# Kernel optimization log

Hardware: AMD Instinct MI355X
Metric: run time of the kernel (lower is better)

## Reference

```python
import math
import jax, jax.numpy as jnp
import numpy as np
from jax import lax

PI = math.pi

def _gauss1d(ks, sigma):
    # kornia gaussian: centered at (ks-1)/2 for both odd and even ks
    x = jnp.arange(ks, dtype=jnp.float32) - (ks - 1) / 2.0
    g = jnp.exp(-0.5 * (x / sigma) ** 2)
    return g / g.sum()

def _unfold_nonoverlap(x, k):
    # F.unfold(x, kernel_size=k, stride=k) for x (B,1,H,W), H,W divisible by k
    B, C, H, W = x.shape
    nH, nW = H // k, W // k
    p = x.reshape(B, nH, k, nW, k).transpose(0, 2, 4, 1, 3)
    return p.reshape(B, k * k, nH * nW)

def _sift(x, ps, nab=8, nsb=4, clipval=0.2, eps=1e-10):
    # kornia SIFTDescriptor(patch_size=ps), x: (N,1,ps,ps) -> (N,128)
    N = x.shape[0]
    g1 = _gauss1d(ps, ps / math.sqrt(2.0))
    gk = jnp.outer(g1, g1)  # (ps,ps), sum 1
    # spatial_gradient mode='diff', normalized, replicate pad
    xp = jnp.pad(x, ((0, 0), (0, 0), (0, 0), (1, 1)), mode='edge')
    gx = 0.5 * (xp[..., 2:] - xp[..., :-2])
    yp = jnp.pad(x, ((0, 0), (0, 0), (1, 1), (0, 0)), mode='edge')
    gy = 0.5 * (yp[:, :, 2:, :] - yp[:, :, :-2, :])
    mag = jnp.sqrt(gx * gx + gy * gy + eps) * gk  # (N,1,ps,ps)
    ori = jnp.arctan2(gy, gx + eps) + 2.0 * PI
    o_big = nab * ori / (2.0 * PI)
    bo0f = jnp.floor(o_big)
    w1 = o_big - bo0f
    bo0 = bo0f.astype(jnp.int32) % nab
    bo1 = (bo0 + 1) % nab
    c0 = jax.nn.one_hot(bo0[:, 0], nab, axis=1, dtype=x.dtype)  # (N,8,ps,ps)
    c1 = jax.nn.one_hot(bo1[:, 0], nab, axis=1, dtype=x.dtype)
    bins = c0 * ((1.0 - w1) * mag) + c1 * (w1 * mag)  # (N,8,ps,ps)
    # triangular pooling kernel, depthwise conv over the 8 angular bins
    bk = 2 * (ps // (nsb + 1)); stride = ps // nsb; pad = bk // 4
    half = bk / 2.0
    xc2 = half - jnp.abs(jnp.arange(bk, dtype=jnp.float32) + 0.5 - half)
    pk = jnp.outer(xc2, xc2) / (half * half)
    pk = jnp.tile(pk[None, None], (nab, 1, 1, 1))  # (8,1,bk,bk)
    pooled = lax.conv_general_dilated(bins, pk, (stride, stride),
        [(pad, pad), (pad, pad)], feature_group_count=nab,
        dimension_numbers=('NCHW', 'OIHW', 'NCHW'))  # (N,8,4,4)
    d = pooled.reshape(N, -1)
    d = d / jnp.maximum(jnp.linalg.norm(d, axis=1, keepdims=True), 1e-12)
    d = jnp.clip(d, 0.0, clipval)
    d = d / jnp.maximum(jnp.linalg.norm(d, axis=1, keepdims=True), 1e-12)
    d = jnp.sqrt(d / jnp.maximum(jnp.abs(d).sum(1, keepdims=True), 1e-12) + eps)  # rootsift
    return d

def _conv_t(x, w, b, stride=2, pad=1):
    # torch ConvTranspose2d; w: (Cin,Cout,k,k)
    k = w.shape[-1]
    wT = jnp.transpose(jnp.flip(w, (-2, -1)), (1, 0, 2, 3))  # (Cout,Cin,k,k)
    y = lax.conv_general_dilated(x, wT, (1, 1),
        [(k - 1 - pad, k - 1 - pad)] * 2, lhs_dilation=(stride, stride),
        dimension_numbers=('NCHW', 'OIHW', 'NCHW'))
    return y + b[None, :, None, None]

def _gn(x, groups, w, b, eps=1e-5):
    N, C, H, W = x.shape
    xg = x.reshape(N, groups, -1)
    mean = xg.mean(-1, keepdims=True)
    var = ((xg - mean) ** 2).mean(-1, keepdims=True)
    xn = ((xg - mean) * lax.rsqrt(var + eps)).reshape(N, C, H, W)
    return xn * w[None, :, None, None] + b[None, :, None, None]

def _jbf(x, guide, ky, kx, sigma_color, sy, sx):
    # kornia joint_bilateral_blur, border='reflect', color_distance='l1'
    B, C, H, W = x.shape
    py, px = ky // 2, kx // 2
    xp = jnp.pad(x, ((0, 0), (0, 0), (py, py), (px, px)), mode='reflect')
    gp = jnp.pad(guide, ((0, 0), (0, 0), (py, py), (px, px)), mode='reflect')
    def win(p):
        return jnp.stack([p[:, :, i:i + H, j:j + W] for i in range(ky) for j in range(kx)], axis=-1)
    ux, ug = win(xp), win(gp)  # (B,C,H,W,ky*kx)
    diff = ug - guide[..., None]
    cd2 = jnp.square(jnp.sum(jnp.abs(diff), axis=1, keepdims=True))
    ck = jnp.exp((-0.5 / (sigma_color ** 2)) * cd2)  # (B,1,H,W,K)
    sk = jnp.outer(_gauss1d(ky, sy), _gauss1d(kx, sx)).reshape(1, 1, 1, 1, -1)
    kern = sk * ck
    return (ux * kern).sum(-1) / kern.sum(-1)

def _forward(x, d1w, d1b, g1w, g1b, s1w, s1b, d2w, d2b, g2w, g2b, s2w, s2b,
             d3w, d3b, g3w, g3b, d4w, d4b, g4w, g4b, fw, fb):
    B = x.shape[0]
    s7 = _sift(_unfold_nonoverlap(x, 7).reshape(-1, 1, 32, 32), 32).reshape(B, 128, 7, 7)
    h = jax.nn.relu(_gn(_conv_t(s7, d1w, d1b), 8, g1w, g1b))  # (B,32,14,14); dropout=identity (eval)
    s14 = _sift(_unfold_nonoverlap(x, 14).reshape(-1, 1, 16, 16), 16).reshape(B, 128, 14, 14)
    sk1 = jnp.einsum('bchw,oc->bohw', s14, s1w[:, :, 0, 0]) + s1b[None, :, None, None]
    h = jax.nn.relu(_gn(_conv_t(jnp.concatenate([h, sk1], 1), d2w, d2b), 4, g2w, g2b))  # (B,16,28,28)
    s28 = _sift(_unfold_nonoverlap(x, 28).reshape(-1, 1, 8, 8), 8).reshape(B, 128, 28, 28)
    sk2 = jnp.einsum('bchw,oc->bohw', s28, s2w[:, :, 0, 0]) + s2b[None, :, None, None]
    h = jax.nn.relu(_gn(_conv_t(jnp.concatenate([h, sk2], 1), d3w, d3b), 2, g3w, g3b))  # (B,8,56,56)
    h = jax.nn.relu(_gn(_conv_t(h, d4w, d4b), 1, g4w, g4b))  # (B,4,112,112)
    h = _conv_t(h, fw, fb)  # (B,2,224,224)
    h = _jbf(h, jnp.tile(x, (1, 2, 1, 1)), 5, 5, 0.1, 1.5, 1.5)
    scale = jnp.array([0.436, 0.615], dtype=h.dtype)
    return jnp.tanh(h) * scale[None, :, None, None]

def setup_inputs() -> dict:
    key = jax.random.key(0)
    ks = jax.random.split(key, 8)
    B = 16
    f32 = jnp.float32
    def rn(k, shp, s=0.05):
        return jax.random.normal(k, shp, f32) * s
    return {
        'x': jax.random.uniform(ks[0], (B, 1, 224, 224), f32),
        'd1w': rn(ks[1], (128, 32, 4, 4)), 'd1b': jnp.zeros((32,), f32),
        'g1w': jnp.ones((32,), f32), 'g1b': jnp.zeros((32,), f32),
        's1w': rn(ks[2], (32, 128, 1, 1)), 's1b': jnp.zeros((32,), f32),
        'd2w': rn(ks[3], (64, 16, 4, 4)), 'd2b': jnp.zeros((16,), f32),
        'g2w': jnp.ones((16,), f32), 'g2b': jnp.zeros((16,), f32),
        's2w': rn(ks[4], (16, 128, 1, 1)), 's2b': jnp.zeros((16,), f32),
        'd3w': rn(ks[5], (32, 8, 4, 4)), 'd3b': jnp.zeros((8,), f32),
        'g3w': jnp.ones((8,), f32), 'g3b': jnp.zeros((8,), f32),
        'd4w': rn(ks[6], (8, 4, 4, 4)), 'd4b': jnp.zeros((4,), f32),
        'g4w': jnp.ones((4,), f32), 'g4b': jnp.zeros((4,), f32),
        'fw': rn(ks[7], (4, 2, 4, 4)), 'fb': jnp.zeros((2,), f32),
    }

def reference(x, d1w, d1b, g1w, g1b, s1w, s1b, d2w, d2b, g2w, g2b, s2w, s2b,
              d3w, d3b, g3w, g3b, d4w, d4b, g4w, g4b, fw, fb):
    return _forward(x, d1w, d1b, g1w, g1b, s1w, s1b, d2w, d2b, g2w, g2b, s2w, s2b,
                    d3w, d3b, g3w, g3b, d4w, d4b, g4w, g4b, fw, fb)
```

## Files before the change

kernel.cpp:

```cpp
#include <hip/hip_runtime.h>
#include <math.h>

#define PI_F 3.14159265358979323846f

template<int PS, int K, int NT>
__global__ __launch_bounds__(NT)
void sift_kernel(const float* __restrict__ x, float* __restrict__ out)
{
    constexpr int NPIX = PS*PS;
    constexpr int BK = 2*(PS/5);
    constexpr int STRIDE = PS/4;
    constexpr int PAD = BK/4;
    constexpr float HALF = BK*0.5f;

    __shared__ float patch[NPIX];
    __shared__ float bins[8*NPIX];
    __shared__ float g1[PS];
    __shared__ float desc[128];
    __shared__ float red[NT];
    __shared__ float gsum_s;

    const int tid = threadIdx.x;
    const int n = blockIdx.x;
    const int b = n / (K*K);
    const int c = n % (K*K);
    const int ki = c / K;
    const int kj = c % K;

    const float* xb = x + (size_t)b*224*224;
    for (int idx = tid; idx < NPIX; idx += NT) {
        int i = idx / PS, j = idx - i*PS;
        patch[idx] = xb[(i*K + ki)*224 + (j*K + kj)];
    }
    if (tid < PS) {
        const float sigma = (float)PS * 0.70710678118654752440f;
        float xv = (float)tid - (PS-1)*0.5f;
        float t = xv / sigma;
        g1[tid] = expf(-0.5f*t*t);
    }
    for (int idx = tid; idx < 8*NPIX; idx += NT) bins[idx] = 0.f;
    __syncthreads();
    if (tid == 0) {
        float s = 0.f;
        for (int i = 0; i < PS; i++) s += g1[i];
        gsum_s = s;
    }
    __syncthreads();
    const float ginv = 1.0f / (gsum_s*gsum_s);

    for (int idx = tid; idx < NPIX; idx += NT) {
        int i = idx / PS, j = idx - i*PS;
        int jm = j > 0 ? j-1 : 0, jp = j < PS-1 ? j+1 : PS-1;
        int im = i > 0 ? i-1 : 0, ip = i < PS-1 ? i+1 : PS-1;
        float gx = 0.5f*(patch[i*PS+jp] - patch[i*PS+jm]);
        float gy = 0.5f*(patch[ip*PS+j] - patch[im*PS+j]);
        float mag = sqrtf(gx*gx + gy*gy + 1e-10f) * (g1[i]*g1[j]*ginv);
        float ori = atan2f(gy, gx + 1e-10f) + 2.f*PI_F;
        float obig = ori * (8.f/(2.f*PI_F));
        float bo0f = floorf(obig);
        float w1 = obig - bo0f;
        int bo0 = ((int)bo0f) & 7;
        int bo1 = (bo0 + 1) & 7;
        bins[bo0*NPIX + idx] = (1.f - w1)*mag;
        bins[bo1*NPIX + idx] = w1*mag;
    }
    __syncthreads();

    for (int t = tid; t < 128; t += NT) {
        int o = t >> 4;
        int py = (t >> 2) & 3;
        int px = t & 3;
        int sy = py*STRIDE - PAD;
        int sx = px*STRIDE - PAD;
        const float* bo = bins + o*NPIX;
        float acc = 0.f;
        for (int di = 0; di < BK; di++) {
            int i = sy + di;
            if (i < 0 || i >= PS) continue;
            float wi = HALF - fabsf((float)di + 0.5f - HALF);
            for (int dj = 0; dj < BK; dj++) {
                int j = sx + dj;
                if (j < 0 || j >= PS) continue;
                float wj = HALF - fabsf((float)dj + 0.5f - HALF);
                acc += bo[i*PS + j] * (wi*wj);
            }
        }
        desc[t] = acc * (1.0f/(HALF*HALF));
    }
    __syncthreads();

    float d = (tid < 128) ? desc[tid] : 0.f;
    red[tid] = d*d; __syncthreads();
    for (int s = NT/2; s > 0; s >>= 1) { if (tid < s) red[tid] += red[tid+s]; __syncthreads(); }
    float nrm = sqrtf(red[0]); __syncthreads();
    d = d / fmaxf(nrm, 1e-12f);
    d = fminf(fmaxf(d, 0.f), 0.2f);
    red[tid] = d*d; __syncthreads();
    for (int s = NT/2; s > 0; s >>= 1) { if (tid < s) red[tid] += red[tid+s]; __syncthreads(); }
    nrm = sqrtf(red[0]); __syncthreads();
    d = d / fmaxf(nrm, 1e-12f);
    red[tid] = d; __syncthreads();
    for (int s = NT/2; s > 0; s >>= 1) { if (tid < s) red[tid] += red[tid+s]; __syncthreads(); }
    float ssum = red[0];
    d = sqrtf(d / fmaxf(ssum, 1e-12f) + 1e-10f);
    if (tid < 128) out[(size_t)n*128 + tid] = d;
}

template<int CIN0, int CIN1, int COUT, int G, int HIN, int NCH, int RT, int NT,
         bool FUSE, int GIN, int NGIN, int NBLK_IN, int NBLK_OUT>
__global__ __launch_bounds__(NT)
void convt_tiled(const float* __restrict__ in0, const float* __restrict__ in1,
                 const float* __restrict__ w, const float* __restrict__ bias,
                 const float2* __restrict__ pst_in,
                 const float* __restrict__ gnw, const float* __restrict__ gnb,
                 float* __restrict__ out, float2* __restrict__ pst_out)
{
    constexpr int CIN = CIN0 + CIN1;
    constexpr int CG = COUT / G;
    constexpr int NGRP = NCH / CG;
    constexpr int CB = COUT / NCH;
    constexpr int H0 = 2*HIN;
    constexpr int SP = H0*H0;
    constexpr int HIN2 = HIN*HIN;
    constexpr int NR = RT/2 + 2;
    constexpr int WIN = HIN + 2;
    constexpr int TILE = CIN*NR*WIN;
    constexpr int WSTRIDE = CIN*NCH*4 + 4;
    constexpr int NPOS = RT*H0;
    constexpr int NWAVE = NT/64;

    __shared__ float tile[TILE];
    __shared__ float wl2[4*WSTRIDE];
    __shared__ float a_s[CIN0];
    __shared__ float b_s[CIN0];
    __shared__ float wpart[NWAVE][NGRP][2];

    const int tid = threadIdx.x;
    const int by = blockIdx.y;
    const int bx = blockIdx.x;
    const int b  = by / CB;
    const int cb = by - b*CB;
    const int c0 = cb*NCH;
    const int g0 = c0 / CG;
    const int r0 = bx * RT;
    const int row0 = r0/2 - 1;

    if constexpr (FUSE) {
        if (tid < CIN0) {
            int gi = tid / (CIN0/GIN);
            float s0 = 0.f, s1 = 0.f;
            for (int k = 0; k < NBLK_IN; k++) {
                float2 p = pst_in[((size_t)b*GIN + gi)*NBLK_IN + k];
                s0 += p.x; s1 += p.y;
            }
            float mean = s0 * (1.f/NGIN);
            float var  = s1 * (1.f/NGIN) - mean*mean;
            float inv  = rsqrtf(var + 1e-5f);
            float a = inv * gnw[tid];
            a_s[tid] = a;
            b_s[tid] = gnb[tid] - mean*a;
        }
        __syncthreads();
    }

    for (int idx = tid; idx < 4*CIN*NCH*4; idx += NT) {
        int k = idx & 3;
        int t2 = idx >> 2;
        int j = t2 % NCH; t2 /= NCH;
        int ci = t2 % CIN;
        int pq = t2 / CIN;
        int pA = pq >> 1, qA = pq & 1;
        int dy = pA + 2*(k>>1), dx = qA + 2*(k&1);
        wl2[pq*WSTRIDE + (ci*NCH + j)*4 + k] = w[(ci*COUT + c0 + j)*16 + dy*4 + dx];
    }

    const float* i0 = in0 + (size_t)b*CIN0*HIN2;
    for (int idx = tid; idx < TILE; idx += NT) {
        int c = idx % WIN;
        int t2 = idx / WIN;
        int r = t2 % NR;
        int ci = t2 / NR;
        int iy = row0 + r, ix = c - 1;
        float v = 0.f;
        if (iy >= 0 && iy < HIN && ix >= 0 && ix < HIN) {
            if (CIN1 == 0 || ci < CIN0) {
                v = i0[ci*HIN2 + iy*HIN + ix];
                if constexpr (FUSE) v = fmaxf(v*a_s[ci] + b_s[ci], 0.f);
            } else {
                v = in1[((size_t)b*CIN1 + (ci-CIN0))*HIN2 + iy*HIN + ix];
            }
        }
        tile[idx] = v;
    }
    __syncthreads();

    float acc[NCH];
    #pragma unroll
    for (int j = 0; j < NCH; j++) acc[j] = 0.f;

    const bool active = tid < NPOS;
    if (active) {
        int oy = r0 + tid / H0, ox = tid % H0;
        int pA = (oy+1)&1, qA = (ox+1)&1;
        int iyA = (oy+1-pA)>>1, ixA = (ox+1-qA)>>1;
        int rA = iyA - row0;
        int cA = ixA + 1;
        int toff = rA*WIN + cA;
        const float* wbase = wl2 + (pA*2+qA)*WSTRIDE;

        #pragma unroll
        for (int j = 0; j < NCH; j++) acc[j] = bias[c0 + j];

        #pragma unroll 4
        for (int ci = 0; ci < CIN; ci++) {
            const float* tp = tile + ci*(NR*WIN) + toff;
            float l0 = tp[0];
            float l1 = tp[-1];
            float l2 = tp[-WIN];
            float l3 = tp[-WIN-1];
            const float* wr = wbase + ci*NCH*4;
            #pragma unroll
            for (int j = 0; j < NCH; j++) {
                const float4 wv = *(const float4*)(wr + j*4);
                acc[j] += l0*wv.x + l1*wv.y + l2*wv.z + l3*wv.w;
            }
        }
        float* ob = out + ((size_t)b*COUT + c0)*SP + r0*H0 + tid;
        #pragma unroll
        for (int j = 0; j < NCH; j++) ob[j*SP] = acc[j];
    }

    const int wv = tid >> 6;
    const int ln = tid & 63;
    #pragma unroll
    for (int grp = 0; grp < NGRP; grp++) {
        float ps = 0.f, pq2 = 0.f;
        #pragma unroll
        for (int j = 0; j < CG; j++) {
            float v = active ? acc[grp*CG + j] : 0.f;
            ps += v; pq2 += v*v;
        }
        #pragma unroll
        for (int off = 32; off > 0; off >>= 1) {
            ps  += __shfl_down(ps,  off);
            pq2 += __shfl_down(pq2, off);
        }
        if (ln == 0) { wpart[wv][grp][0] = ps; wpart[wv][grp][1] = pq2; }
    }
    __syncthreads();
    if (tid < NGRP) {
        float s0 = 0.f, s1 = 0.f;
        #pragma unroll
        for (int w2 = 0; w2 < NWAVE; w2++) { s0 += wpart[w2][tid][0]; s1 += wpart[w2][tid][1]; }
        pst_out[((size_t)b*G + g0 + tid)*NBLK_OUT + bx] = make_float2(s0, s1);
    }
}

template<int CO, int S>
__global__ __launch_bounds__(256)
void conv1x1(const float* __restrict__ in, const float* __restrict__ w,
             const float* __restrict__ bias, float* __restrict__ out)
{
    __shared__ float wt[128*CO];
    const int tid = threadIdx.x;
    for (int i = tid; i < 128*CO; i += 256) {
        int c = i / CO, co = i - c*CO;
        wt[i] = w[co*128 + c];
    }
    __syncthreads();
    int idx = blockIdx.x*256 + tid;
    int s = idx % S; int r = idx / S;
    int co4 = r % (CO/4); int b = r / (CO/4);
    int co = co4*4;
    const float* ib = in + (size_t)b*128*S + s;
    float acc0 = bias[co], acc1 = bias[co+1], acc2 = bias[co+2], acc3 = bias[co+3];
    #pragma unroll 8
    for (int c = 0; c < 128; c++) {
        float v = ib[c*S];
        const float4 wv = *(const float4*)&wt[c*CO + co];
        acc0 += v*wv.x; acc1 += v*wv.y; acc2 += v*wv.z; acc3 += v*wv.w;
    }
    float* ob = out + ((size_t)b*CO + co)*S + s;
    ob[0] = acc0; ob[S] = acc1; ob[2*S] = acc2; ob[3*S] = acc3;
}

__global__ __launch_bounds__(256)
void convt_final_fused(const float* __restrict__ in, const float* __restrict__ w,
                       const float* __restrict__ bias,
                       const float2* __restrict__ pst_in,
                       const float* __restrict__ gnw, const float* __restrict__ gnb,
                       float* __restrict__ out)
{
    __shared__ float wl2[128];
    __shared__ float a_s[4], b_s[4], bl[2], mv[2];
    const int tid = threadIdx.x;
    const int b = blockIdx.y;
    if (tid < 128) {
        int k = tid & 3;
        int t = tid >> 2;
        int co = t & 1; t >>= 1;
        int ci = t & 3;
        int pq = t >> 2;
        int pA = pq >> 1, qA = pq & 1;
        int dy = pA + 2*(k>>1), dx = qA + 2*(k&1);
        wl2[tid] = w[(ci*2 + co)*16 + dy*4 + dx];
    }
    if (tid < 2) bl[tid] = bias[tid];
    if (tid < 64) {
        float s0 = 0.f, s1 = 0.f;
        for (int k = tid; k < 56; k += 64) {
            float2 p = pst_in[(size_t)b*56 + k];
            s0 += p.x; s1 += p.y;
        }
        #pragma unroll
        for (int off = 32; off > 0; off >>= 1) {
            s0 += __shfl_down(s0, off);
            s1 += __shfl_down(s1, off);
        }
        if (tid == 0) {
            float mean = s0 * (1.f/50176.f);
            float var  = s1 * (1.f/50176.f) - mean*mean;
            mv[0] = mean;
            mv[1] = rsqrtf(var + 1e-5f);
        }
    }
    __syncthreads();
    if (tid < 4) {
        float a = mv[1] * gnw[tid];
        a_s[tid] = a;
        b_s[tid] = gnb[tid] - mv[0]*a;
    }
    __syncthreads();

    int e = blockIdx.x*256 + tid;
    int oy = e / 224, ox = e - oy*224;
    int pA = (oy+1)&1, iyA = (oy+1-pA)>>1, iyB = iyA-1;
    int qA = (ox+1)&1, ixA = (ox+1-qA)>>1, ixB = ixA-1;
    float mYA = (iyA < 112) ? 1.f : 0.f;
    float mYB = (iyB >= 0)  ? 1.f : 0.f;
    float mXA = (ixA < 112) ? 1.f : 0.f;
    float mXB = (ixB >= 0)  ? 1.f : 0.f;
    float m0 = mYA*mXA, m1 = mYA*mXB, m2 = mYB*mXA, m3 = mYB*mXB;
    int iyAc = min(iyA, 111), iyBc = max(iyB, 0);
    int ixAc = min(ixA, 111), ixBc = max(ixB, 0);
    int oAA = iyAc*112 + ixAc, oAB = iyAc*112 + ixBc;
    int oBA = iyBc*112 + ixAc, oBB = iyBc*112 + ixBc;
    const float* wbase = wl2 + (pA*2+qA)*32;

    float acc0 = bl[0], acc1 = bl[1];
    const float* ib = in + (size_t)b*4*112*112;
    #pragma unroll
    for (int ci = 0; ci < 4; ci++) {
        const float* ip = ib + ci*112*112;
        float a = a_s[ci], bb = b_s[ci];
        float l0 = fmaxf(ip[oAA]*a + bb, 0.f);
        float l1 = fmaxf(ip[oAB]*a + bb, 0.f);
        float l2 = fmaxf(ip[oBA]*a + bb, 0.f);
        float l3 = fmaxf(ip[oBB]*a + bb, 0.f);
        float t0 = l0*m0, t1 = l1*m1, t2 = l2*m2, t3 = l3*m3;
        const float4 w0 = *(const float4*)(wbase + ci*8);
        const float4 w1 = *(const float4*)(wbase + ci*8 + 4);
        acc0 += t0*w0.x + t1*w0.y + t2*w0.z + t3*w0.w;
        acc1 += t0*w1.x + t1*w1.y + t2*w1.z + t3*w1.w;
    }
    float* ob = out + (size_t)b*2*50176 + e;
    ob[0] = acc0;
    ob[50176] = acc1;
}

__global__ __launch_bounds__(256)
void bilateral_tanh(const float* __restrict__ x, const float* __restrict__ pre,
                    float* __restrict__ out)
{
    const float g[5] = {0.1200783f, 0.2338817f, 0.2920800f, 0.2338817f, 0.1200783f};
    int idx = blockIdx.x*256 + threadIdx.x;
    int px = idx % 224; int r = idx / 224;
    int py = r % 224; int b = r / 224;
    int s = py*224 + px;
    const float* xb = x + (size_t)b*50176;
    const float* p0 = pre + (size_t)b*2*50176;
    const float* p1 = p0 + 50176;
    float center = xb[s];
    float wsum = 0.f, a0 = 0.f, a1 = 0.f;
    #pragma unroll
    for (int di = -2; di <= 2; di++){
        int yy = py + di; yy = yy < 0 ? -yy : (yy > 223 ? 446 - yy : yy);
        #pragma unroll
        for (int dj = -2; dj <= 2; dj++){
            int xx = px + dj; xx = xx < 0 ? -xx : (xx > 223 ? 446 - xx : xx);
            int o = yy*224 + xx;
            float dg = xb[o] - center;
            float wgt = g[di+2]*g[dj+2]*__expf(-200.f*dg*dg);
            wsum += wgt;
            a0 += wgt * p0[o];
            a1 += wgt * p1[o];
        }
    }
    float inv = 1.0f / wsum;
    out[(size_t)(b*2)*50176 + s]     = tanhf(a0*inv)*0.436f;
    out[(size_t)(b*2+1)*50176 + s]   = tanhf(a1*inv)*0.615f;
}

extern "C" void kernel_launch(void* const* d_in, const int* in_sizes, int n_in,
                              void* d_out, int out_size, void* d_ws, size_t ws_size,
                              hipStream_t stream) {
    (void)in_sizes; (void)n_in; (void)out_size; (void)ws_size;
    const float* x   = (const float*)d_in[0];
    const float* d1w = (const float*)d_in[1];
    const float* d1b = (const float*)d_in[2];
    const float* g1w = (const float*)d_in[3];
    const float* g1b = (const float*)d_in[4];
    const float* s1w = (const float*)d_in[5];
    const float* s1b = (const float*)d_in[6];
    const float* d2w = (const float*)d_in[7];
    const float* d2b = (const float*)d_in[8];
    const float* g2w = (const float*)d_in[9];
    const float* g2b = (const float*)d_in[10];
    const float* s2w = (const float*)d_in[11];
    const float* s2b = (const float*)d_in[12];
    const float* d3w = (const float*)d_in[13];
    const float* d3b = (const float*)d_in[14];
    const float* g3w = (const float*)d_in[15];
    const float* g3b = (const float*)d_in[16];
    const float* d4w = (const float*)d_in[17];
    const float* d4b = (const float*)d_in[18];
    const float* g4w = (const float*)d_in[19];
    const float* g4b = (const float*)d_in[20];
    const float* fw  = (const float*)d_in[21];
    const float* fb  = (const float*)d_in[22];
    float* out = (float*)d_out;

    float* ws  = (float*)d_ws;
    float* s7  = ws;
    float* s14 = s7  + 100352;
    float* s28 = s14 + 401408;
    float* h1  = s28 + 1605632;
    float* sk1 = h1  + 100352;
    float* h2  = sk1 + 100352;
    float* sk2 = h2  + 200704;
    float* h3  = sk2 + 200704;
    float* h4  = h3  + 401408;
    float* pre = h4  + 802816;
    float2* pst1 = (float2*)(pre + 1605632);
    float2* pst2 = pst1 + 128;
    float2* pst3 = pst2 + 448;
    float2* pst4 = pst3 + 448;

    sift_kernel<32, 7, 256><<<784,   256, 0, stream>>>(x, s7);
    sift_kernel<16,14, 256><<<3136,  256, 0, stream>>>(x, s14);
    sift_kernel< 8,28, 128><<<12544, 128, 0, stream>>>(x, s28);

    conv1x1<32, 196><<<98,  256, 0, stream>>>(s14, s1w, s1b, sk1);
    conv1x1<16, 784><<<196, 256, 0, stream>>>(s28, s2w, s2b, sk2);

    convt_tiled<128, 0, 32, 8,  7, 4, 14, 256, false, 1, 1, 1, 1>
        <<<dim3(1, 16*8), 256, 0, stream>>>(s7, nullptr, d1w, d1b, nullptr, nullptr, nullptr, h1, pst1);
    convt_tiled< 32,32, 16, 4, 14, 8,  4, 128, true, 8, 784, 1, 7>
        <<<dim3(7, 16*2), 128, 0, stream>>>(h1, sk1, d2w, d2b, pst1, g1w, g1b, h2, pst2);
    convt_tiled< 16,16,  8, 2, 28, 8,  4, 256, true, 4, 3136, 7, 14>
        <<<dim3(14, 16), 256, 0, stream>>>(h2, sk2, d3w, d3b, pst2, g2w, g2b, h3, pst3);
    convt_tiled<  8, 0,  4, 1, 56, 4,  2, 256, true, 2, 12544, 14, 56>
        <<<dim3(56, 16), 256, 0, stream>>>(h3, nullptr, d4w, d4b, pst3, g3w, g3b, h4, pst4);

    convt_final_fused<<<dim3(196, 16), 256, 0, stream>>>(h4, fw, fb, pst4, g4w, g4b, pre);
    bilateral_tanh<<<3136, 256, 0, stream>>>(x, pre, out);
}
```

Before: 270.0 us.

## Use wave-shuffle reductions in SIFT, split pooling rows, tile bilateral filter in LDS

The SIFT kernel's three tree reductions, which each needed a barrier per step, become wave shuffles followed by a small cross-wave sum, cutting barrier count. For 256-thread blocks the pooling step splits its rows across two halves of the block so all threads do work. The bilateral filter now stages a 20x20 halo tile of x and both pre channels in shared memory instead of issuing 75 global loads per pixel. The workspace buffers are also reordered, which is layout-neutral.

```diff
diff --git a/kernel.cpp b/kernel.cpp
--- a/kernel.cpp
+++ b/kernel.cpp
@@ -12,12 +12,15 @@
     constexpr int STRIDE = PS/4;
     constexpr int PAD = BK/4;
     constexpr float HALF = BK*0.5f;
+    constexpr int NWAVE = NT/64;
+    constexpr int HALVES = (NT >= 256) ? 2 : 1;
+    constexpr int ROWS = BK / HALVES;
 
     __shared__ float patch[NPIX];
     __shared__ float bins[8*NPIX];
     __shared__ float g1[PS];
-    __shared__ float desc[128];
-    __shared__ float red[NT];
+    __shared__ float pool2[128];
+    __shared__ float wred[NWAVE];
     __shared__ float gsum_s;
 
     const int tid = threadIdx.x;
@@ -66,15 +69,18 @@
     }
     __syncthreads();
 
-    for (int t = tid; t < 128; t += NT) {
+    float pacc = 0.f;
+    const int t = tid & 127;
+    const int half = (HALVES == 2) ? (tid >> 7) : 0;
+    if (tid < 128*HALVES) {
         int o = t >> 4;
         int py = (t >> 2) & 3;
         int px = t & 3;
         int sy = py*STRIDE - PAD;
         int sx = px*STRIDE - PAD;
         const float* bo = bins + o*NPIX;
-        float acc = 0.f;
-        for (int di = 0; di < BK; di++) {
+        for (int dr = 0; dr < ROWS; dr++) {
+            int di = half*ROWS + dr;
             int i = sy + di;
             if (i < 0 || i >= PS) continue;
             float wi = HALF - fabsf((float)di + 0.5f - HALF);
@@ -82,28 +88,88 @@
                 int j = sx + dj;
                 if (j < 0 || j >= PS) continue;
                 float wj = HALF - fabsf((float)dj + 0.5f - HALF);
-                acc += bo[i*PS + j] * (wi*wj);
+                pacc += bo[i*PS + j] * (wi*wj);
             }
         }
-        desc[t] = acc * (1.0f/(HALF*HALF));
-    }
-    __syncthreads();
-
-    float d = (tid < 128) ? desc[tid] : 0.f;
-    red[tid] = d*d; __syncthreads();
-    for (int s = NT/2; s > 0; s >>= 1) { if (tid < s) red[tid] += red[tid+s]; __syncthreads(); }
-    float nrm = sqrtf(red[0]); __syncthreads();
+    }
+    if (HALVES == 2) {
+        if (half == 1) pool2[t] = pacc;
+        __syncthreads();
+    }
+    float d = 0.f;
+    if (tid < 128) {
+        d = pacc;
+        if (HALVES == 2) d += pool2[tid];
+        d *= 1.0f/(HALF*HALF);
+    }
+
+    const int wv = tid >> 6;
+    const int ln = tid & 63;
+
+    float v = d*d;
+    #pragma unroll
+    for (int off = 32; off > 0; off >>= 1) v += __shfl_down(v, off);
+    if (ln == 0) wred[wv] = v;
+    __syncthreads();
+    float nrm = 0.f;
+    #pragma unroll
+    for (int w2 = 0; w2 < NWAVE; w2++) nrm += wred[w2];
+    nrm = sqrtf(nrm);
+    __syncthreads();
     d = d / fmaxf(nrm, 1e-12f);
     d = fminf(fmaxf(d, 0.f), 0.2f);
-    red[tid] = d*d; __syncthreads();
-    for (int s = NT/2; s > 0; s >>= 1) { if (tid < s) red[tid] += red[tid+s]; __syncthreads(); }
-    nrm = sqrtf(red[0]); __syncthreads();
+
+    v = d*d;
+    #pragma unroll
+    for (int off = 32; off > 0; off >>= 1) v += __shfl_down(v, off);
+    if (ln == 0) wred[wv] = v;
+    __syncthreads();
+    nrm = 0.f;
+    #pragma unroll
+    for (int w2 = 0; w2 < NWAVE; w2++) nrm += wred[w2];
+    nrm = sqrtf(nrm);
+    __syncthreads();
     d = d / fmaxf(nrm, 1e-12f);
-    red[tid] = d; __syncthreads();
-    for (int s = NT/2; s > 0; s >>= 1) { if (tid < s) red[tid] += red[tid+s]; __syncthreads(); }
-    float ssum = red[0];
+
+    v = d;
+    #pragma unroll
+    for (int off = 32; off > 0; off >>= 1) v += __shfl_down(v, off);
+    if (ln == 0) wred[wv] = v;
+    __syncthreads();
+    float ssum = 0.f;
+    #pragma unroll
+    for (int w2 = 0; w2 < NWAVE; w2++) ssum += wred[w2];
     d = sqrtf(d / fmaxf(ssum, 1e-12f) + 1e-10f);
+
     if (tid < 128) out[(size_t)n*128 + tid] = d;
+}
+
+template<int CO, int S>
+__global__ __launch_bounds__(256)
+void conv1x1(const float* __restrict__ in, const float* __restrict__ w,
+             const float* __restrict__ bias, float* __restrict__ out)
+{
+    __shared__ float wt[128*CO];
+    const int tid = threadIdx.x;
+    for (int i = tid; i < 128*CO; i += 256) {
+        int c = i / CO, co = i - c*CO;
+        wt[i] = w[co*128 + c];
+    }
+    __syncthreads();
+    int idx = blockIdx.x*256 + tid;
+    int s = idx % S; int r = idx / S;
+    int co4 = r % (CO/4); int b = r / (CO/4);
+    int co = co4*4;
+    const float* ib = in + (size_t)b*128*S + s;
+    float acc0 = bias[co], acc1 = bias[co+1], acc2 = bias[co+2], acc3 = bias[co+3];
+    #pragma unroll 8
+    for (int c = 0; c < 128; c++) {
+        float v = ib[c*S];
+        const float4 wv = *(const float4*)&wt[c*CO + co];
+        acc0 += v*wv.x; acc1 += v*wv.y; acc2 += v*wv.z; acc3 += v*wv.w;
+    }
+    float* ob = out + ((size_t)b*CO + co)*S + s;
+    ob[0] = acc0; ob[S] = acc1; ob[2*S] = acc2; ob[3*S] = acc3;
 }
 
 template<int CIN0, int CIN1, int COUT, int G, int HIN, int NCH, int RT, int NT,
@@ -256,34 +322,6 @@
     }
 }
 
-template<int CO, int S>
-__global__ __launch_bounds__(256)
-void conv1x1(const float* __restrict__ in, const float* __restrict__ w,
-             const float* __restrict__ bias, float* __restrict__ out)
-{
-    __shared__ float wt[128*CO];
-    const int tid = threadIdx.x;
-    for (int i = tid; i < 128*CO; i += 256) {
-        int c = i / CO, co = i - c*CO;
-        wt[i] = w[co*128 + c];
-    }
-    __syncthreads();
-    int idx = blockIdx.x*256 + tid;
-    int s = idx % S; int r = idx / S;
-    int co4 = r % (CO/4); int b = r / (CO/4);
-    int co = co4*4;
-    const float* ib = in + (size_t)b*128*S + s;
-    float acc0 = bias[co], acc1 = bias[co+1], acc2 = bias[co+2], acc3 = bias[co+3];
-    #pragma unroll 8
-    for (int c = 0; c < 128; c++) {
-        float v = ib[c*S];
-        const float4 wv = *(const float4*)&wt[c*CO + co];
-        acc0 += v*wv.x; acc1 += v*wv.y; acc2 += v*wv.z; acc3 += v*wv.w;
-    }
-    float* ob = out + ((size_t)b*CO + co)*S + s;
-    ob[0] = acc0; ob[S] = acc1; ob[2*S] = acc2; ob[3*S] = acc3;
-}
-
 __global__ __launch_bounds__(256)
 void convt_final_fused(const float* __restrict__ in, const float* __restrict__ w,
                        const float* __restrict__ bias,
@@ -369,34 +407,49 @@
 }
 
 __global__ __launch_bounds__(256)
-void bilateral_tanh(const float* __restrict__ x, const float* __restrict__ pre,
-                    float* __restrict__ out)
+void bilateral_tiled(const float* __restrict__ x, const float* __restrict__ pre,
+                     float* __restrict__ out)
 {
     const float g[5] = {0.1200783f, 0.2338817f, 0.2920800f, 0.2338817f, 0.1200783f};
-    int idx = blockIdx.x*256 + threadIdx.x;
-    int px = idx % 224; int r = idx / 224;
-    int py = r % 224; int b = r / 224;
-    int s = py*224 + px;
+    __shared__ float xs[400], p0s[400], p1s[400];
+
+    const int tid = threadIdx.x;
+    const int b = blockIdx.z;
+    const int ty0 = blockIdx.y*16;
+    const int tx0 = blockIdx.x*16;
     const float* xb = x + (size_t)b*50176;
     const float* p0 = pre + (size_t)b*2*50176;
     const float* p1 = p0 + 50176;
-    float center = xb[s];
+
+    for (int idx = tid; idx < 400; idx += 256) {
+        int r = idx / 20, cc = idx - r*20;
+        int gy = ty0 - 2 + r;  gy = gy < 0 ? -gy : (gy > 223 ? 446 - gy : gy);
+        int gx = tx0 - 2 + cc; gx = gx < 0 ? -gx : (gx > 223 ? 446 - gx : gx);
+        int o = gy*224 + gx;
+        xs[idx]  = xb[o];
+        p0s[idx] = p0[o];
+        p1s[idx] = p1[o];
+    }
+    __syncthreads();
+
+    int ly = tid >> 4, lx = tid & 15;
+    int base = (ly+2)*20 + (lx+2);
+    float center = xs[base];
     float wsum = 0.f, a0 = 0.f, a1 = 0.f;
     #pragma unroll
     for (int di = -2; di <= 2; di++){
-        int yy = py + di; yy = yy < 0 ? -yy : (yy > 223 ? 446 - yy : yy);
         #pragma unroll
         for (int dj = -2; dj <= 2; dj++){
-            int xx = px + dj; xx = xx < 0 ? -xx : (xx > 223 ? 446 - xx : xx);
-            int o = yy*224 + xx;
-            float dg = xb[o] - center;
+            int o = base + di*20 + dj;
+            float dg = xs[o] - center;
             float wgt = g[di+2]*g[dj+2]*__expf(-200.f*dg*dg);
             wsum += wgt;
-            a0 += wgt * p0[o];
-            a1 += wgt * p1[o];
+            a0 += wgt * p0s[o];
+            a1 += wgt * p1s[o];
         }
     }
     float inv = 1.0f / wsum;
+    int s = (ty0 + ly)*224 + (tx0 + lx);
     out[(size_t)(b*2)*50176 + s]     = tanhf(a0*inv)*0.436f;
     out[(size_t)(b*2+1)*50176 + s]   = tanhf(a1*inv)*0.615f;
 }
@@ -434,11 +487,11 @@
     float* s7  = ws;
     float* s14 = s7  + 100352;
     float* s28 = s14 + 401408;
-    float* h1  = s28 + 1605632;
-    float* sk1 = h1  + 100352;
-    float* h2  = sk1 + 100352;
-    float* sk2 = h2  + 200704;
-    float* h3  = sk2 + 200704;
+    float* sk1 = s28 + 1605632;
+    float* sk2 = sk1 + 100352;
+    float* h1  = sk2 + 200704;
+    float* h2  = h1  + 100352;
+    float* h3  = h2  + 200704;
     float* h4  = h3  + 401408;
     float* pre = h4  + 802816;
     float2* pst1 = (float2*)(pre + 1605632);
@@ -463,5 +516,5 @@
         <<<dim3(56, 16), 256, 0, stream>>>(h3, nullptr, d4w, d4b, pst3, g3w, g3b, h4, pst4);
 
     convt_final_fused<<<dim3(196, 16), 256, 0, stream>>>(h4, fw, fb, pst4, g4w, g4b, pre);
-    bilateral_tanh<<<3136, 256, 0, stream>>>(x, pre, out);
+    bilateral_tiled<<<dim3(14, 14, 16), 256, 0, stream>>>(x, pre, out);
 }
```

Result: faster. 247.5 us (-8.3%).
